# Kernel tuning notes

Measured on AMD Instinct MI355X. Metric: run time of the kernel, lower is better.

The kernel has to match this reference:

```python
import jax, jax.numpy as jnp
import numpy as np

N_UNITS = 1024
H = 16
D_HEAD = N_UNITS // H
D_FF = 4 * N_UNITS
BATCH = 8
SEQ = 1024
EPS = 1e-3


def setup_inputs() -> dict:
    key = jax.random.key(0)
    ks = jax.random.split(key, 12)
    s = 3.0 / N_UNITS  # LinearSent init scale (not math-relevant, just realistic)
    sf = 3.0 / D_FF
    return {
        "e": jax.random.normal(ks[0], (BATCH, N_UNITS, SEQ), dtype=jnp.float32),
        "xx_mask": jnp.ones((BATCH, SEQ, SEQ), dtype=bool),
        "W_Q": jax.random.uniform(ks[1], (N_UNITS, N_UNITS), minval=-s, maxval=s),
        "W_K": jax.random.uniform(ks[2], (N_UNITS, N_UNITS), minval=-s, maxval=s),
        "W_V": jax.random.uniform(ks[3], (N_UNITS, N_UNITS), minval=-s, maxval=s),
        "W_O": jax.random.uniform(ks[4], (N_UNITS, N_UNITS), minval=-s, maxval=s),
        "W_1": jax.random.uniform(ks[5], (D_FF, N_UNITS), minval=-s, maxval=s),
        "b_1": jnp.zeros((D_FF,), dtype=jnp.float32),
        "W_2": jax.random.uniform(ks[6], (N_UNITS, D_FF), minval=-sf, maxval=sf),
        "b_2": jnp.zeros((N_UNITS,), dtype=jnp.float32),
        "ln1_a": jnp.ones((N_UNITS,), dtype=jnp.float32),
        "ln1_b": jnp.zeros((N_UNITS,), dtype=jnp.float32),
        "ln2_a": jnp.ones((N_UNITS,), dtype=jnp.float32),
        "ln2_b": jnp.zeros((N_UNITS,), dtype=jnp.float32),
    }


def _layer_norm_sent(z, a, b):
    # z: (B, U, L). Torch LayerNorm normalizes over dim=1 (units) with
    # unbiased std: (z - mu) / (std + eps) * a + b
    mu = jnp.mean(z, axis=1, keepdims=True)
    sigma = jnp.std(z, axis=1, keepdims=True, ddof=1)
    return (z - mu) / (sigma + EPS) * a[None, :, None] + b[None, :, None]


def _mha(e, mask, W_Q, W_K, W_V, W_O):
    b, u, L = e.shape
    scale = 1.0 / np.sqrt(D_HEAD)
    # projections: (B, U, L); chunk along units into H heads of D_HEAD
    Q = jnp.einsum("ou,bul->bol", W_Q, e).reshape(b, H, D_HEAD, L)
    K = jnp.einsum("ou,bul->bol", W_K, e).reshape(b, H, D_HEAD, L)
    V = jnp.einsum("ou,bul->bol", W_V, e).reshape(b, H, D_HEAD, L)
    scores = jnp.einsum("bhdq,bhdk->bhqk", Q, K) * scale
    scores = jnp.where(mask[:, None, :, :], scores, -jnp.inf)
    A = jax.nn.softmax(scores, axis=-1)
    A = jnp.where(jnp.isnan(A), 0.0, A)  # fully-masked rows -> 0 (as in torch)
    C = jnp.einsum("bhqk,bhdk->bhdq", A, V).reshape(b, u, L)
    return jnp.einsum("ou,bul->bol", W_O, C)


def reference(e, xx_mask, W_Q, W_K, W_V, W_O, W_1, b_1, W_2, b_2,
              ln1_a, ln1_b, ln2_a, ln2_b):
    # self-attention + residual + LayerNormSent (dropout = identity in eval)
    e = e + _mha(e, xx_mask, W_Q, W_K, W_V, W_O)
    e = _layer_norm_sent(e, ln1_a, ln1_b)
    # position-wise FFN: W_2 @ relu(W_1 @ e + b_1) + b_2
    h = jax.nn.relu(jnp.einsum("fu,bul->bfl", W_1, e) + b_1[None, :, None])
    ffn = jnp.einsum("uf,bfl->bul", W_2, h) + b_2[None, :, None]
    e = e + ffn
    e = _layer_norm_sent(e, ln2_a, ln2_b)
    return e
```

## Files before the change

kernel.cpp:

```cpp
#include <hip/hip_runtime.h>
#include <stdint.h>

typedef float f32x4 __attribute__((ext_vector_type(4)));
typedef short s16x8 __attribute__((ext_vector_type(8)));
typedef short s16x4 __attribute__((ext_vector_type(4)));

#define B_  8
#define U_  1024
#define L_  1024
#define H_  16
#define DH_ 64
#define FF_ 4096
#define EPS_ 1e-3f

__device__ __forceinline__ short f2bf(float f){
  union { float f; uint32_t u; } x; x.f = f;
  uint32_t r = x.u + 0x7fffu + ((x.u >> 16) & 1u);
  return (short)(r >> 16);
}

__device__ __forceinline__ float bf2f(short s){
  union { uint32_t u; float f; } x; x.u = ((uint32_t)(uint16_t)s) << 16;
  return x.f;
}

__device__ __forceinline__ uint32_t cvtpk(float lo, float hi){
  uint32_t r;
  asm("v_cvt_pk_bf16_f32 %0, %1, %2" : "=v"(r) : "v"(lo), "v"(hi));
  return r;
}

__global__ __launch_bounds__(256) void castk(const float* __restrict__ in,
                                             short* __restrict__ out, int n4){
  int i = blockIdx.x * 256 + threadIdx.x;
  if (i < n4){
    f32x4 v = ((const f32x4*)in)[i];
    s16x4 o;
    o[0]=f2bf(v[0]); o[1]=f2bf(v[1]); o[2]=f2bf(v[2]); o[3]=f2bf(v[3]);
    ((s16x4*)out)[i] = o;
  }
}

__global__ __launch_bounds__(256) void transpose_e(const float* __restrict__ e,
                                                   short* __restrict__ etb){
  __shared__ float tile[32][33];
  int b = blockIdx.z;
  int u0 = blockIdx.x * 32, l0 = blockIdx.y * 32;
  int tx = threadIdx.x & 31, ty = threadIdx.x >> 5;
  const float* src = e + ((size_t)b * U_ + u0) * L_ + l0;
  #pragma unroll
  for (int k = 0; k < 32; k += 8) tile[ty + k][tx] = src[(size_t)(ty + k) * L_ + tx];
  __syncthreads();
  short* dstb = etb + ((size_t)b * L_ + l0) * U_ + u0;
  #pragma unroll
  for (int k = 0; k < 32; k += 8)
    dstb[(size_t)(ty + k) * U_ + tx] = f2bf(tile[tx][ty + k]);
}

__device__ __forceinline__ void gload16(const void* g, void* l){
  __builtin_amdgcn_global_load_lds((const __attribute__((address_space(1))) void*)g,
                                   (__attribute__((address_space(3))) void*)l, 16, 0, 0);
}

template<int MODE>
__global__ __launch_bounds__(256)
void gemm_bt(const short* __restrict__ A, int lda, long long strideA,
             const short* __restrict__ Bt, int ldb, long long strideB,
             int K,
             void* __restrict__ Out, int ldo, long long strideO)
{
  int b = blockIdx.z;
  const short* Ab = A  + (size_t)b * strideA;
  const short* Bb = Bt + (size_t)b * strideB;
  int m0 = blockIdx.x * 128, n0 = blockIdx.y * 128;
  __shared__ short As[128 * 64];
  __shared__ short Bs[128 * 64];
  int tid = threadIdx.x;
  int lane = tid & 63, wid = tid >> 6;
  int wm = (wid >> 1) * 64, wn = (wid & 1) * 64;
  int r16 = lane & 15, g4 = lane >> 4;
  f32x4 acc[4][4] = {};

  for (int k0 = 0; k0 < K; k0 += 64) {
    #pragma unroll
    for (int it = 0; it < 4; ++it) {
      int idx = it * 256 + tid;
      int row = idx >> 3, c8 = idx & 7;
      int gc = c8 ^ (row & 7);
      gload16(Ab + (size_t)(m0 + row) * lda + k0 + gc * 8, &As[idx * 8]);
    }
    #pragma unroll
    for (int it = 0; it < 4; ++it) {
      int idx = it * 256 + tid;
      int row = idx >> 3, c8 = idx & 7;
      int gc = c8 ^ (row & 7);
      gload16(Bb + (size_t)(n0 + row) * ldb + k0 + gc * 8, &Bs[idx * 8]);
    }
    __syncthreads();

    s16x8 af[4][2], bf[4][2];
    #pragma unroll
    for (int m = 0; m < 4; ++m)
      #pragma unroll
      for (int s = 0; s < 2; ++s){
        int row = wm + m * 16 + r16;
        int c = (s * 4 + g4) ^ (row & 7);
        af[m][s] = *(const s16x8*)&As[row * 64 + c * 8];
      }
    #pragma unroll
    for (int n = 0; n < 4; ++n)
      #pragma unroll
      for (int s = 0; s < 2; ++s){
        int row = wn + n * 16 + r16;
        int c = (s * 4 + g4) ^ (row & 7);
        bf[n][s] = *(const s16x8*)&Bs[row * 64 + c * 8];
      }
    #pragma unroll
    for (int m = 0; m < 4; ++m)
      #pragma unroll
      for (int n = 0; n < 4; ++n)
        #pragma unroll
        for (int s = 0; s < 2; ++s)
          acc[m][n] = __builtin_amdgcn_mfma_f32_16x16x32_bf16(af[m][s], bf[n][s], acc[m][n], 0, 0, 0);
    __syncthreads();
  }

  #pragma unroll
  for (int m = 0; m < 4; ++m)
    #pragma unroll
    for (int n = 0; n < 4; ++n)
      #pragma unroll
      for (int r = 0; r < 4; ++r){
        int gr = m0 + wm + m * 16 + g4 * 4 + r;
        int gc = n0 + wn + n * 16 + r16;
        ((short*)Out)[(size_t)b * strideO + (size_t)gr * ldo + gc] = f2bf(acc[m][n][r]);
      }
}

__device__ __forceinline__ void stage_half8(const short* __restrict__ A,
    const short* __restrict__ Bt, int lda, int ldb, int m0, int n0, int k0,
    short* As, short* Bs, int H, int tid)
{
  const short* src; short* dst; int ld, gbase;
  if (H < 2){ src = A;  dst = As + H * 128 * 64; ld = lda; gbase = m0 + H * 128; }
  else      { src = Bt; dst = Bs + (H - 2) * 128 * 64; ld = ldb; gbase = n0 + (H - 2) * 128; }
  #pragma unroll
  for (int j = 0; j < 2; ++j){
    int idx = j * 512 + tid;
    int rl = idx >> 3, c8 = idx & 7;
    int gc = c8 ^ (rl & 7);
    gload16(src + (size_t)(gbase + rl) * ld + k0 + gc * 8, dst + idx * 8);
  }
}

#define RAWBAR() asm volatile("s_barrier" ::: "memory")
#define VMCNT2() asm volatile("s_waitcnt vmcnt(2)" ::: "memory")

template<int MODE>
__global__ __launch_bounds__(512, 2)
void gemm8(const short* __restrict__ A, int lda,
           const short* __restrict__ Bt, int ldb, int K,
           void* __restrict__ Out, int ldo,
           const float* __restrict__ bias, int NTL)
{
  __shared__ short As[2][256 * 64];
  __shared__ short Bs[2][256 * 64];
  int id = blockIdx.x;
  int xcd = id & 7, j = id >> 3;
  int nt = j & ((1 << NTL) - 1);
  int mt = xcd * 4 + (j >> NTL);
  int m0 = mt * 256, n0 = nt * 256;
  int tid = threadIdx.x, lane = tid & 63, wid = tid >> 6;
  int wr = wid >> 2, wc = wid & 3;
  int r16 = lane & 15, g4 = lane >> 4;
  int NT = K >> 6;

  f32x4 acc[8][4] = {};

  stage_half8(A, Bt, lda, ldb, m0, n0, 0,  (short*)As[0], (short*)Bs[0], 0, tid);
  stage_half8(A, Bt, lda, ldb, m0, n0, 0,  (short*)As[0], (short*)Bs[0], 1, tid);
  stage_half8(A, Bt, lda, ldb, m0, n0, 0,  (short*)As[0], (short*)Bs[0], 2, tid);
  stage_half8(A, Bt, lda, ldb, m0, n0, 0,  (short*)As[0], (short*)Bs[0], 3, tid);
  stage_half8(A, Bt, lda, ldb, m0, n0, 64, (short*)As[1], (short*)Bs[1], 0, tid);
  VMCNT2();
  RAWBAR();

  for (int t = 0; t < NT; ++t){
    int c = t & 1;
    short* Asc = (short*)As[c];     short* Bsc = (short*)Bs[c];
    short* Asn = (short*)As[c ^ 1]; short* Bsn = (short*)Bs[c ^ 1];
    int kn1 = (t + 1) << 6, kn2 = (t + 2) << 6;
    bool h1 = (t + 1 < NT), h2 = (t + 2 < NT);
    s16x8 af[8], bfr[4];

    #pragma unroll
    for (int m = 0; m < 8; ++m){
      int row = wr * 128 + m * 16 + r16;
      af[m] = *(const s16x8*)&Asc[row * 64 + (g4 ^ (row & 7)) * 8];
    }
    #pragma unroll
    for (int n = 0; n < 4; ++n){
      int row = wc * 64 + n * 16 + r16;
      bfr[n] = *(const s16x8*)&Bsc[row * 64 + (g4 ^ (row & 7)) * 8];
    }
    if (h1) stage_half8(A, Bt, lda, ldb, m0, n0, kn1, Asn, Bsn, 1, tid);
    RAWBAR();
    __builtin_amdgcn_s_setprio(1);
    #pragma unroll
    for (int m = 0; m < 8; ++m){
      acc[m][0] = __builtin_amdgcn_mfma_f32_16x16x32_bf16(af[m], bfr[0], acc[m][0], 0, 0, 0);
      acc[m][1] = __builtin_amdgcn_mfma_f32_16x16x32_bf16(af[m], bfr[1], acc[m][1], 0, 0, 0);
    }
    __builtin_amdgcn_s_setprio(0);
    RAWBAR();

    if (h1) stage_half8(A, Bt, lda, ldb, m0, n0, kn1, Asn, Bsn, 2, tid);
    RAWBAR();
    __builtin_amdgcn_s_setprio(1);
    #pragma unroll
    for (int m = 0; m < 8; ++m){
      acc[m][2] = __builtin_amdgcn_mfma_f32_16x16x32_bf16(af[m], bfr[2], acc[m][2], 0, 0, 0);
      acc[m][3] = __builtin_amdgcn_mfma_f32_16x16x32_bf16(af[m], bfr[3], acc[m][3], 0, 0, 0);
    }
    __builtin_amdgcn_s_setprio(0);
    RAWBAR();

    #pragma unroll
    for (int m = 0; m < 8; ++m){
      int row = wr * 128 + m * 16 + r16;
      af[m] = *(const s16x8*)&Asc[row * 64 + ((4 + g4) ^ (row & 7)) * 8];
    }
    #pragma unroll
    for (int n = 0; n < 4; ++n){
      int row = wc * 64 + n * 16 + r16;
      bfr[n] = *(const s16x8*)&Bsc[row * 64 + ((4 + g4) ^ (row & 7)) * 8];
    }
    if (h1) stage_half8(A, Bt, lda, ldb, m0, n0, kn1, Asn, Bsn, 3, tid);
    RAWBAR();
    __builtin_amdgcn_s_setprio(1);
    #pragma unroll
    for (int m = 0; m < 8; ++m){
      acc[m][0] = __builtin_amdgcn_mfma_f32_16x16x32_bf16(af[m], bfr[0], acc[m][0], 0, 0, 0);
      acc[m][1] = __builtin_amdgcn_mfma_f32_16x16x32_bf16(af[m], bfr[1], acc[m][1], 0, 0, 0);
    }
    __builtin_amdgcn_s_setprio(0);
    RAWBAR();

    if (h2) stage_half8(A, Bt, lda, ldb, m0, n0, kn2, Asc, Bsc, 0, tid);
    RAWBAR();
    __builtin_amdgcn_s_setprio(1);
    #pragma unroll
    for (int m = 0; m < 8; ++m){
      acc[m][2] = __builtin_amdgcn_mfma_f32_16x16x32_bf16(af[m], bfr[2], acc[m][2], 0, 0, 0);
      acc[m][3] = __builtin_amdgcn_mfma_f32_16x16x32_bf16(af[m], bfr[3], acc[m][3], 0, 0, 0);
    }
    __builtin_amdgcn_s_setprio(0);
    VMCNT2();
    RAWBAR();
  }

  #pragma unroll
  for (int m = 0; m < 8; ++m)
    #pragma unroll
    for (int n = 0; n < 4; ++n)
      #pragma unroll
      for (int r = 0; r < 4; ++r){
        int gr = m0 + wr * 128 + m * 16 + g4 * 4 + r;
        int gc = n0 + wc * 64 + n * 16 + r16;
        float v = acc[m][n][r];
        if (MODE == 0){
          ((short*)Out)[(size_t)gr * ldo + gc] = f2bf(v);
        } else {
          float z = v + bias[gc]; z = z > 0.f ? z : 0.f;
          ((short*)Out)[(size_t)gr * ldo + gc] = f2bf(z);
        }
      }
}

__device__ __forceinline__ void stage_n(const short* __restrict__ A,
    const short* __restrict__ Bt, int lda, int ldb, int m0, int n0, int k0,
    short* As, short* Bs, int H, int tid)
{
  const short* src; short* dst; int ld, gbase;
  if (H < 2){ src = A;  dst = As + H * 128 * 64; ld = lda; gbase = m0 + H * 128; }
  else      { src = Bt; dst = Bs; ld = ldb; gbase = n0; }
  #pragma unroll
  for (int j = 0; j < 2; ++j){
    int idx = j * 512 + tid;
    int rl = idx >> 3, c8 = idx & 7;
    int gc = c8 ^ (rl & 7);
    gload16(src + (size_t)(gbase + rl) * ld + k0 + gc * 8, dst + idx * 8);
  }
}

template<int MODE>
__global__ __launch_bounds__(512, 2)
void gemm8n(const short* __restrict__ A, int lda,
            const short* __restrict__ Bt, int ldb, int K,
            float* __restrict__ Out, int ldo,
            const float* __restrict__ bias,
            const short* __restrict__ resb, int ldr, int NTL)
{
  __shared__ short As[2][256 * 64];
  __shared__ short Bs[2][128 * 64];
  int id = blockIdx.x;
  int xcd = id & 7, j = id >> 3;
  int nt = j & ((1 << NTL) - 1);
  int mt = xcd * 4 + (j >> NTL);
  int m0 = mt * 256, n0 = nt * 128;
  int tid = threadIdx.x, lane = tid & 63, wid = tid >> 6;
  int wr = wid >> 1, wc = wid & 1;
  int r16 = lane & 15, g4 = lane >> 4;
  int NT = K >> 6;

  f32x4 acc[4][4] = {};

  stage_n(A, Bt, lda, ldb, m0, n0, 0,  (short*)As[0], (short*)Bs[0], 0, tid);
  stage_n(A, Bt, lda, ldb, m0, n0, 0,  (short*)As[0], (short*)Bs[0], 1, tid);
  stage_n(A, Bt, lda, ldb, m0, n0, 0,  (short*)As[0], (short*)Bs[0], 2, tid);
  stage_n(A, Bt, lda, ldb, m0, n0, 64, (short*)As[1], (short*)Bs[1], 0, tid);
  VMCNT2();
  RAWBAR();

  for (int t = 0; t < NT; ++t){
    int c = t & 1;
    short* Asc = (short*)As[c];     short* Bsc = (short*)Bs[c];
    short* Asn = (short*)As[c ^ 1]; short* Bsn = (short*)Bs[c ^ 1];
    int kn1 = (t + 1) << 6, kn2 = (t + 2) << 6;
    bool h1 = (t + 1 < NT), h2 = (t + 2 < NT);
    s16x8 af[4], bfr[4];

    #pragma unroll
    for (int m = 0; m < 4; ++m){
      int row = wr * 64 + m * 16 + r16;
      af[m] = *(const s16x8*)&Asc[row * 64 + (g4 ^ (row & 7)) * 8];
    }
    #pragma unroll
    for (int n = 0; n < 4; ++n){
      int row = wc * 64 + n * 16 + r16;
      bfr[n] = *(const s16x8*)&Bsc[row * 64 + (g4 ^ (row & 7)) * 8];
    }
    if (h1) stage_n(A, Bt, lda, ldb, m0, n0, kn1, Asn, Bsn, 1, tid);
    RAWBAR();
    __builtin_amdgcn_s_setprio(1);
    #pragma unroll
    for (int m = 0; m < 4; ++m){
      acc[m][0] = __builtin_amdgcn_mfma_f32_16x16x32_bf16(af[m], bfr[0], acc[m][0], 0, 0, 0);
      acc[m][1] = __builtin_amdgcn_mfma_f32_16x16x32_bf16(af[m], bfr[1], acc[m][1], 0, 0, 0);
    }
    __builtin_amdgcn_s_setprio(0);
    RAWBAR();

    if (h1) stage_n(A, Bt, lda, ldb, m0, n0, kn1, Asn, Bsn, 2, tid);
    RAWBAR();
    __builtin_amdgcn_s_setprio(1);
    #pragma unroll
    for (int m = 0; m < 4; ++m){
      acc[m][2] = __builtin_amdgcn_mfma_f32_16x16x32_bf16(af[m], bfr[2], acc[m][2], 0, 0, 0);
      acc[m][3] = __builtin_amdgcn_mfma_f32_16x16x32_bf16(af[m], bfr[3], acc[m][3], 0, 0, 0);
    }
    __builtin_amdgcn_s_setprio(0);
    RAWBAR();

    #pragma unroll
    for (int m = 0; m < 4; ++m){
      int row = wr * 64 + m * 16 + r16;
      af[m] = *(const s16x8*)&Asc[row * 64 + ((4 + g4) ^ (row & 7)) * 8];
    }
    #pragma unroll
    for (int n = 0; n < 4; ++n){
      int row = wc * 64 + n * 16 + r16;
      bfr[n] = *(const s16x8*)&Bsc[row * 64 + ((4 + g4) ^ (row & 7)) * 8];
    }
    RAWBAR();
    __builtin_amdgcn_s_setprio(1);
    #pragma unroll
    for (int m = 0; m < 4; ++m){
      acc[m][0] = __builtin_amdgcn_mfma_f32_16x16x32_bf16(af[m], bfr[0], acc[m][0], 0, 0, 0);
      acc[m][1] = __builtin_amdgcn_mfma_f32_16x16x32_bf16(af[m], bfr[1], acc[m][1], 0, 0, 0);
    }
    __builtin_amdgcn_s_setprio(0);
    RAWBAR();

    if (h2) stage_n(A, Bt, lda, ldb, m0, n0, kn2, Asc, Bsc, 0, tid);
    RAWBAR();
    __builtin_amdgcn_s_setprio(1);
    #pragma unroll
    for (int m = 0; m < 4; ++m){
      acc[m][2] = __builtin_amdgcn_mfma_f32_16x16x32_bf16(af[m], bfr[2], acc[m][2], 0, 0, 0);
      acc[m][3] = __builtin_amdgcn_mfma_f32_16x16x32_bf16(af[m], bfr[3], acc[m][3], 0, 0, 0);
    }
    __builtin_amdgcn_s_setprio(0);
    VMCNT2();
    RAWBAR();
  }

  #pragma unroll
  for (int m = 0; m < 4; ++m)
    #pragma unroll
    for (int n = 0; n < 4; ++n)
      #pragma unroll
      for (int r = 0; r < 4; ++r){
        int gr = m0 + wr * 64 + m * 16 + g4 * 4 + r;
        int gc = n0 + wc * 64 + n * 16 + r16;
        float v = acc[m][n][r];
        float rv = bf2f(resb[(size_t)gr * ldr + gc]);
        if (MODE == 1){
          Out[(size_t)gr * ldo + gc] = v + rv;
        } else {
          Out[(size_t)gr * ldo + gc] = v + bias[gc] + rv;
        }
      }
}

__global__ __launch_bounds__(256)
void attn_kernel(const short* __restrict__ QKt,
                 const short* __restrict__ Vd, short* __restrict__ Ct)
{
  int bh = blockIdx.x;
  int b = bh >> 4, h = bh & 15;
  int qt = blockIdx.y;
  int tid = threadIdx.x, lane = tid & 63, w = tid >> 6;
  int r16 = lane & 15, g4 = lane >> 4;
  int hd = h * 64;
  const float cs = 0.125f * 1.44269504089f;
  const int LDQ = 2048;

  __shared__ short Ks[2][64 * 64];
  __shared__ short Vs[2][64 * 64];

  const short* Qb = QKt + (size_t)b * L_ * LDQ;
  const short* Kb = Qb + 1024;
  const short* Vb = Vd + (size_t)b * U_ * L_;

  s16x8 aq[2][2];
  #pragma unroll
  for (int m = 0; m < 2; ++m)
    #pragma unroll
    for (int s = 0; s < 2; ++s){
      int qrow = qt * 128 + w * 32 + m * 16 + r16;
      aq[m][s] = *(const s16x8*)&Qb[(size_t)qrow * LDQ + hd + s * 32 + g4 * 8];
    }

  f32x4 o[2][4] = {};
  float mr[2] = {0.f, 0.f};
  float lr[2] = {0.f, 0.f};

  int srow = tid >> 3, sc8 = tid & 7;
  int sgc0 = sc8 ^ (srow & 7);
  int srow1 = (256 + tid) >> 3;
  int sgc1 = sc8 ^ (srow1 & 7);

  #define STAGE(buf, kb_) do {                                                  \
    int k0s = (kb_) * 64;                                                       \
    gload16(Kb + (size_t)(k0s + srow ) * LDQ + hd + sgc0 * 8, &Ks[buf][(tid      ) * 8]); \
    gload16(Kb + (size_t)(k0s + srow1) * LDQ + hd + sgc1 * 8, &Ks[buf][(256 + tid) * 8]); \
    gload16(Vb + (size_t)(hd + srow ) * L_ + k0s + sgc0 * 8, &Vs[buf][(tid      ) * 8]); \
    gload16(Vb + (size_t)(hd + srow1) * L_ + k0s + sgc1 * 8, &Vs[buf][(256 + tid) * 8]); \
  } while (0)

  STAGE(0, 0);
  __syncthreads();
  int cur = 0;

  int a_lo = (((lane >> 4) & 1) << 7) + ((lane & 15) << 2);

  for (int kb = 0; kb < 16; ++kb){
    if (kb + 1 < 16) STAGE(cur ^ 1, kb + 1);

    s16x8 ak[4][2];
    #pragma unroll
    for (int nt = 0; nt < 4; ++nt)
      #pragma unroll
      for (int s = 0; s < 2; ++s){
        int row = nt * 16 + r16;
        int c = (s * 4 + g4) ^ (row & 7);
        ak[nt][s] = *(const s16x8*)&Ks[cur][row * 64 + c * 8];
      }
    f32x4 st[2][4];
    __builtin_amdgcn_s_setprio(1);
    #pragma unroll
    for (int m = 0; m < 2; ++m)
      #pragma unroll
      for (int nt = 0; nt < 4; ++nt){
        f32x4 a = {};
        #pragma unroll
        for (int s = 0; s < 2; ++s)
          a = __builtin_amdgcn_mfma_f32_16x16x32_bf16(ak[nt][s], aq[m][s], a, 0, 0, 0);
        st[m][nt] = a;
      }
    __builtin_amdgcn_s_setprio(0);

    s16x8 bv[4][2];
    #pragma unroll
    for (int nt2 = 0; nt2 < 4; ++nt2)
      #pragma unroll
      for (int s = 0; s < 2; ++s){
        int row = nt2 * 16 + r16;
        int c = (s * 4 + g4) ^ (row & 7);
        bv[nt2][s] = *(const s16x8*)&Vs[cur][row * 64 + c * 8];
      }

    #pragma unroll
    for (int m = 0; m < 2; ++m){
      float t0 = fmaxf(fmaxf(st[m][0][0], st[m][0][1]), fmaxf(st[m][0][2], st[m][0][3]));
      float t1 = fmaxf(fmaxf(st[m][1][0], st[m][1][1]), fmaxf(st[m][1][2], st[m][1][3]));
      float t2 = fmaxf(fmaxf(st[m][2][0], st[m][2][1]), fmaxf(st[m][2][2], st[m][2][3]));
      float t3 = fmaxf(fmaxf(st[m][3][0], st[m][3][1]), fmaxf(st[m][3][2], st[m][3][3]));
      float tmax = fmaxf(fmaxf(t0, t1), fmaxf(t2, t3));

      if (!__all(tmax <= mr[m] + 64.f)){
        float tf = tmax;
        tf = fmaxf(tf, __shfl_xor(tf, 16, 64));
        tf = fmaxf(tf, __shfl_xor(tf, 32, 64));
        float mn = fmaxf(mr[m], tf);
        float alpha = exp2f((mr[m] - mn) * cs);
        mr[m] = mn;
        lr[m] *= alpha;
        float ar[4];
        #pragma unroll
        for (int r = 0; r < 4; ++r)
          ar[r] = __shfl(alpha, (lane & 48) | ((((lane >> 4) & 3) * 4 + r) & 15), 64);
        #pragma unroll
        for (int nt2 = 0; nt2 < 4; ++nt2)
          #pragma unroll
          for (int r = 0; r < 4; ++r) o[m][nt2][r] *= ar[r];
      }

      float m2 = mr[m] * cs;
      float p[4][4], ps = 0.f;
      #pragma unroll
      for (int nt = 0; nt < 4; ++nt)
        #pragma unroll
        for (int r = 0; r < 4; ++r){
          float pv = exp2f(st[m][nt][r] * cs - m2);
          p[nt][r] = pv;
          ps += pv;
        }
      lr[m] += ps;

      uint32_t pw[4][2];
      #pragma unroll
      for (int nt = 0; nt < 4; ++nt){
        pw[nt][0] = cvtpk(p[nt][0], p[nt][1]);
        pw[nt][1] = cvtpk(p[nt][2], p[nt][3]);
      }
      union { uint32_t w[4]; s16x8 v; } pa[2];
      #pragma unroll
      for (int s = 0; s < 2; ++s)
        #pragma unroll
        for (int wj = 0; wj < 4; ++wj){
          int addr = a_lo + ((wj >> 1) << 6);
          uint32_t A  = __builtin_amdgcn_ds_bpermute(addr, (int)pw[2 * s    ][wj & 1]);
          uint32_t Bv = __builtin_amdgcn_ds_bpermute(addr, (int)pw[2 * s + 1][wj & 1]);
          pa[s].w[wj] = (lane < 32) ? A : Bv;
        }

      __builtin_amdgcn_s_setprio(1);
      #pragma unroll
      for (int s = 0; s < 2; ++s)
        #pragma unroll
        for (int nt2 = 0; nt2 < 4; ++nt2)
          o[m][nt2] = __builtin_amdgcn_mfma_f32_16x16x32_bf16(pa[s].v, bv[nt2][s], o[m][nt2], 0, 0, 0);
      __builtin_amdgcn_s_setprio(0);
    }

    __syncthreads();
    cur ^= 1;
  }
  #undef STAGE

  short* Cb = Ct + (size_t)b * L_ * U_;
  #pragma unroll
  for (int m = 0; m < 2; ++m){
    float l = lr[m];
    l += __shfl_xor(l, 16, 64);
    l += __shfl_xor(l, 32, 64);
    float linv = 1.f / l;
    float lv[4];
    #pragma unroll
    for (int r = 0; r < 4; ++r)
      lv[r] = __shfl(linv, (lane & 48) | ((((lane >> 4) & 3) * 4 + r) & 15), 64);
    #pragma unroll
    for (int nt2 = 0; nt2 < 4; ++nt2)
      #pragma unroll
      for (int r = 0; r < 4; ++r){
        int q = qt * 128 + w * 32 + m * 16 + g4 * 4 + r;
        float v = o[m][nt2][r] * lv[r];
        Cb[(size_t)q * U_ + hd + nt2 * 16 + r16] = f2bf(v);
      }
  }
}

__global__ __launch_bounds__(256)
void ln_kernel(const float* __restrict__ z, const float* __restrict__ ga,
               const float* __restrict__ gb, short* __restrict__ outb)
{
  int row = blockIdx.x;
  const float* zr = z + (size_t)row * U_;
  int tid = threadIdx.x;
  float v[4];
  float s = 0.f, sq = 0.f;
  #pragma unroll
  for (int i = 0; i < 4; ++i){
    v[i] = zr[tid + i * 256];
    s += v[i]; sq += v[i] * v[i];
  }
  #pragma unroll
  for (int d = 1; d < 64; d <<= 1){
    s  += __shfl_xor(s, d, 64);
    sq += __shfl_xor(sq, d, 64);
  }
  __shared__ float ss[4], ssq[4];
  int w = tid >> 6, lane = tid & 63;
  if (lane == 0){ ss[w] = s; ssq[w] = sq; }
  __syncthreads();
  s  = ss[0] + ss[1] + ss[2] + ss[3];
  sq = ssq[0] + ssq[1] + ssq[2] + ssq[3];
  float mu = s * (1.f / 1024.f);
  float var = (sq - 1024.f * mu * mu) * (1.f / 1023.f);
  var = var > 0.f ? var : 0.f;
  float inv = 1.f / (sqrtf(var) + EPS_);
  #pragma unroll
  for (int i = 0; i < 4; ++i){
    int u = tid + i * 256;
    outb[(size_t)row * U_ + u] = f2bf((v[i] - mu) * inv * ga[u] + gb[u]);
  }
}

__global__ __launch_bounds__(256)
void ln_stats(const float* __restrict__ z, float* __restrict__ st2)
{
  int row = blockIdx.x;
  const float* zr = z + (size_t)row * U_;
  int tid = threadIdx.x;
  float s = 0.f, sq = 0.f;
  #pragma unroll
  for (int i = 0; i < 4; ++i){
    float v = zr[tid + i * 256];
    s += v; sq += v * v;
  }
  #pragma unroll
  for (int d = 1; d < 64; d <<= 1){
    s  += __shfl_xor(s, d, 64);
    sq += __shfl_xor(sq, d, 64);
  }
  __shared__ float ss[4], ssq[4];
  int w = tid >> 6, lane = tid & 63;
  if (lane == 0){ ss[w] = s; ssq[w] = sq; }
  __syncthreads();
  if (tid == 0){
    s  = ss[0] + ss[1] + ss[2] + ss[3];
    sq = ssq[0] + ssq[1] + ssq[2] + ssq[3];
    float mu = s * (1.f / 1024.f);
    float var = (sq - 1024.f * mu * mu) * (1.f / 1023.f);
    var = var > 0.f ? var : 0.f;
    st2[2 * row]     = mu;
    st2[2 * row + 1] = 1.f / (sqrtf(var) + EPS_);
  }
}

__global__ __launch_bounds__(256)
void transpose_ln(const float* __restrict__ z, const float* __restrict__ st2,
                  const float* __restrict__ ga, const float* __restrict__ gb,
                  float* __restrict__ out)
{
  __shared__ float tile[32][33];
  int b = blockIdx.z;
  int l0 = blockIdx.x * 32, u0 = blockIdx.y * 32;
  int tx = threadIdx.x & 31, ty = threadIdx.x >> 5;
  const float* src = z + ((size_t)b * L_ + l0) * U_ + u0;
  #pragma unroll
  for (int k = 0; k < 32; k += 8) tile[ty + k][tx] = src[(size_t)(ty + k) * U_ + tx];
  __syncthreads();
  size_t rbase = (size_t)b * L_ + l0 + tx;
  float mu  = st2[2 * rbase];
  float inv = st2[2 * rbase + 1];
  float* dst = out + ((size_t)b * U_ + u0) * L_ + l0;
  #pragma unroll
  for (int k = 0; k < 32; k += 8){
    int u = u0 + ty + k;
    float v = (tile[tx][ty + k] - mu) * inv * ga[u] + gb[u];
    dst[(size_t)(ty + k) * L_ + tx] = v;
  }
}

extern "C" void kernel_launch(void* const* d_in, const int* in_sizes, int n_in,
                              void* d_out, int out_size, void* d_ws, size_t ws_size,
                              hipStream_t stream)
{
  const float* e    = (const float*)d_in[0];
  const float* W_Q  = (const float*)d_in[2];
  const float* W_K  = (const float*)d_in[3];
  const float* W_V  = (const float*)d_in[4];
  const float* W_O  = (const float*)d_in[5];
  const float* W_1  = (const float*)d_in[6];
  const float* b_1  = (const float*)d_in[7];
  const float* W_2  = (const float*)d_in[8];
  const float* b_2  = (const float*)d_in[9];
  const float* ln1a = (const float*)d_in[10];
  const float* ln1b = (const float*)d_in[11];
  const float* ln2a = (const float*)d_in[12];
  const float* ln2b = (const float*)d_in[13];

  char* ws = (char*)d_ws;
  const size_t MB = 1ull << 20;
  short* wbqk = (short*)(ws + 0 * MB);
  short* wbv  = (short*)(ws + 4 * MB);
  short* wbo  = (short*)(ws + 6 * MB);
  short* wb1  = (short*)(ws + 8 * MB);
  short* wb2  = (short*)(ws + 16 * MB);
  short* etb  = (short*)(ws + 24 * MB);
  float* st2  = (float*)(ws + 56 * MB);
  short* QKt  = (short*)(ws + 72 * MB);
  short* Vd   = (short*)(ws + 104 * MB);
  short* Ct   = (short*)(ws + 120 * MB);
  float* z1t  = (float*)(ws + 72 * MB);
  short* e1b  = (short*)(ws + 104 * MB);
  short* ht   = (short*)(ws + 136 * MB);
  float* z2t  = (float*)(ws + 24 * MB);

  const long long S1M = 1024LL * 1024LL;

  castk<<<1024, 256, 0, stream>>>(W_Q, wbqk, 262144);
  castk<<<1024, 256, 0, stream>>>(W_K, wbqk + 1048576, 262144);
  castk<<<1024, 256, 0, stream>>>(W_V, wbv, 262144);
  castk<<<1024, 256, 0, stream>>>(W_O, wbo, 262144);
  castk<<<4096, 256, 0, stream>>>(W_1, wb1, 1048576);
  castk<<<4096, 256, 0, stream>>>(W_2, wb2, 1048576);

  transpose_e<<<dim3(32, 32, 8), 256, 0, stream>>>(e, etb);

  gemm8<0><<<256, 512, 0, stream>>>(etb, 1024, wbqk, 1024, 1024, QKt, 2048,
                                    nullptr, 3);
  gemm_bt<0><<<dim3(8, 8, 8), 256, 0, stream>>>(wbv, 1024, 0, etb, 1024, S1M, 1024,
                                                Vd, 1024, S1M);

  attn_kernel<<<dim3(128, 8), 256, 0, stream>>>(QKt, Vd, Ct);

  gemm8n<1><<<256, 512, 0, stream>>>(Ct, 1024, wbo, 1024, 1024, z1t, 1024,
                                     nullptr, etb, 1024, 3);
  ln_kernel<<<8192, 256, 0, stream>>>(z1t, ln1a, ln1b, e1b);

  gemm8<2><<<512, 512, 0, stream>>>(e1b, 1024, wb1, 1024, 1024, ht, 4096,
                                    b_1, 4);
  gemm8n<3><<<256, 512, 0, stream>>>(ht, 4096, wb2, 4096, 4096, z2t, 1024,
                                     b_2, e1b, 1024, 3);

  ln_stats<<<8192, 256, 0, stream>>>(z2t, st2);
  transpose_ln<<<dim3(32, 32, 8), 256, 0, stream>>>(z2t, st2, ln2a, ln2b, (float*)d_out);
}
```

Before: 401.6 us.

## Replace V-projection GEMM with pipelined 256x128 kernel and fuse weight casts

The V projection used a simple 128x128 GEMM that staged each k-tile and then synchronised before computing. It is replaced with a 512-thread 256x128 tile kernel that double-buffers LDS through async global-to-LDS loads interleaved with MFMA phases, uses setprio around MFMAs, and orders blocks with XCD-aware indexing. The six separate weight-cast launches are merged into one kernel to cut launch overhead. The new kernel adds more barriers and relies on a stage_n helper defined elsewhere in the file.

Result: faster. 390.8 us (-2.7%).

```diff
diff --git a/kernel.cpp b/kernel.cpp
--- a/kernel.cpp
+++ b/kernel.cpp
@@ -30,15 +30,28 @@
   return r;
 }
 
-__global__ __launch_bounds__(256) void castk(const float* __restrict__ in,
-                                             short* __restrict__ out, int n4){
+__global__ __launch_bounds__(256)
+void castall(const float* __restrict__ wq, const float* __restrict__ wk,
+             const float* __restrict__ wv, const float* __restrict__ wo,
+             const float* __restrict__ w1, const float* __restrict__ w2,
+             short* __restrict__ wbqk, short* __restrict__ wbv,
+             short* __restrict__ wbo, short* __restrict__ wb1,
+             short* __restrict__ wb2)
+{
   int i = blockIdx.x * 256 + threadIdx.x;
-  if (i < n4){
-    f32x4 v = ((const f32x4*)in)[i];
-    s16x4 o;
-    o[0]=f2bf(v[0]); o[1]=f2bf(v[1]); o[2]=f2bf(v[2]); o[3]=f2bf(v[3]);
-    ((s16x4*)out)[i] = o;
-  }
+  const float* src; short* dst; int off;
+  if (i < 524288){
+    if (i < 262144){ src = wq; dst = wbqk;            off = i; }
+    else           { src = wk; dst = wbqk + 1048576;  off = i - 262144; }
+  } else if (i < 1048576){
+    if (i < 786432){ src = wv; dst = wbv; off = i - 524288; }
+    else           { src = wo; dst = wbo; off = i - 786432; }
+  } else if (i < 2097152){ src = w1; dst = wb1; off = i - 1048576; }
+  else                   { src = w2; dst = wb2; off = i - 2097152; }
+  f32x4 v = ((const f32x4*)src)[off];
+  s16x4 o;
+  o[0]=f2bf(v[0]); o[1]=f2bf(v[1]); o[2]=f2bf(v[2]); o[3]=f2bf(v[3]);
+  ((s16x4*)dst)[off] = o;
 }
 
 __global__ __launch_bounds__(256) void transpose_e(const float* __restrict__ e,
@@ -62,80 +75,8 @@
                                    (__attribute__((address_space(3))) void*)l, 16, 0, 0);
 }
 
-template<int MODE>
-__global__ __launch_bounds__(256)
-void gemm_bt(const short* __restrict__ A, int lda, long long strideA,
-             const short* __restrict__ Bt, int ldb, long long strideB,
-             int K,
-             void* __restrict__ Out, int ldo, long long strideO)
-{
-  int b = blockIdx.z;
-  const short* Ab = A  + (size_t)b * strideA;
-  const short* Bb = Bt + (size_t)b * strideB;
-  int m0 = blockIdx.x * 128, n0 = blockIdx.y * 128;
-  __shared__ short As[128 * 64];
-  __shared__ short Bs[128 * 64];
-  int tid = threadIdx.x;
-  int lane = tid & 63, wid = tid >> 6;
-  int wm = (wid >> 1) * 64, wn = (wid & 1) * 64;
-  int r16 = lane & 15, g4 = lane >> 4;
-  f32x4 acc[4][4] = {};
-
-  for (int k0 = 0; k0 < K; k0 += 64) {
-    #pragma unroll
-    for (int it = 0; it < 4; ++it) {
-      int idx = it * 256 + tid;
-      int row = idx >> 3, c8 = idx & 7;
-      int gc = c8 ^ (row & 7);
-      gload16(Ab + (size_t)(m0 + row) * lda + k0 + gc * 8, &As[idx * 8]);
-    }
-    #pragma unroll
-    for (int it = 0; it < 4; ++it) {
-      int idx = it * 256 + tid;
-      int row = idx >> 3, c8 = idx & 7;
-      int gc = c8 ^ (row & 7);
-      gload16(Bb + (size_t)(n0 + row) * ldb + k0 + gc * 8, &Bs[idx * 8]);
-    }
-    __syncthreads();
-
-    s16x8 af[4][2], bf[4][2];
-    #pragma unroll
-    for (int m = 0; m < 4; ++m)
-      #pragma unroll
-      for (int s = 0; s < 2; ++s){
-        int row = wm + m * 16 + r16;
-        int c = (s * 4 + g4) ^ (row & 7);
-        af[m][s] = *(const s16x8*)&As[row * 64 + c * 8];
-      }
-    #pragma unroll
-    for (int n = 0; n < 4; ++n)
-      #pragma unroll
-      for (int s = 0; s < 2; ++s){
-        int row = wn + n * 16 + r16;
-        int c = (s * 4 + g4) ^ (row & 7);
-        bf[n][s] = *(const s16x8*)&Bs[row * 64 + c * 8];
-      }
-    #pragma unroll
-    for (int m = 0; m < 4; ++m)
-      #pragma unroll
-      for (int n = 0; n < 4; ++n)
-        #pragma unroll
-        for (int s = 0; s < 2; ++s)
-          acc[m][n] = __builtin_amdgcn_mfma_f32_16x16x32_bf16(af[m][s], bf[n][s], acc[m][n], 0, 0, 0);
-    __syncthreads();
-  }
-
-  #pragma unroll
-  for (int m = 0; m < 4; ++m)
-    #pragma unroll
-    for (int n = 0; n < 4; ++n)
-      #pragma unroll
-      for (int r = 0; r < 4; ++r){
-        int gr = m0 + wm + m * 16 + g4 * 4 + r;
-        int gc = n0 + wn + n * 16 + r16;
-        ((short*)Out)[(size_t)b * strideO + (size_t)gr * ldo + gc] = f2bf(acc[m][n][r]);
-      }
-}
+#define RAWBAR() asm volatile("s_barrier" ::: "memory")
+#define VMCNT2() asm volatile("s_waitcnt vmcnt(2)" ::: "memory")
 
 __device__ __forceinline__ void stage_half8(const short* __restrict__ A,
     const short* __restrict__ Bt, int lda, int ldb, int m0, int n0, int k0,
@@ -152,9 +93,6 @@
     gload16(src + (size_t)(gbase + rl) * ld + k0 + gc * 8, dst + idx * 8);
   }
 }
-
-#define RAWBAR() asm volatile("s_barrier" ::: "memory")
-#define VMCNT2() asm volatile("s_waitcnt vmcnt(2)" ::: "memory")
 
 template<int MODE>
 __global__ __launch_bounds__(512, 2)
@@ -410,6 +348,120 @@
         } else {
           Out[(size_t)gr * ldo + gc] = v + bias[gc] + rv;
         }
+      }
+}
+
+__global__ __launch_bounds__(512, 2)
+void gemm8b(const short* __restrict__ A,
+            const short* __restrict__ Bt,
+            short* __restrict__ Out)
+{
+  __shared__ short As[2][256 * 64];
+  __shared__ short Bs[2][128 * 64];
+  int id = blockIdx.x;
+  int xcd = id & 7, j = id >> 3;
+  int pair = xcd * 8 + (j >> 2);
+  int mt = j & 3;
+  int b = pair >> 3, nt = pair & 7;
+  int m0 = mt * 256, n0 = nt * 128;
+  const short* Bb = Bt + (size_t)b * 1048576;
+  short* Ob = Out + (size_t)b * 1048576;
+  int tid = threadIdx.x, lane = tid & 63, wid = tid >> 6;
+  int wr = wid >> 1, wc = wid & 1;
+  int r16 = lane & 15, g4 = lane >> 4;
+  const int NT = 16;
+
+  f32x4 acc[4][4] = {};
+
+  stage_n(A, Bb, 1024, 1024, m0, n0, 0,  (short*)As[0], (short*)Bs[0], 0, tid);
+  stage_n(A, Bb, 1024, 1024, m0, n0, 0,  (short*)As[0], (short*)Bs[0], 1, tid);
+  stage_n(A, Bb, 1024, 1024, m0, n0, 0,  (short*)As[0], (short*)Bs[0], 2, tid);
+  stage_n(A, Bb, 1024, 1024, m0, n0, 64, (short*)As[1], (short*)Bs[1], 0, tid);
+  VMCNT2();
+  RAWBAR();
+
+  for (int t = 0; t < NT; ++t){
+    int c = t & 1;
+    short* Asc = (short*)As[c];     short* Bsc = (short*)Bs[c];
+    short* Asn = (short*)As[c ^ 1]; short* Bsn = (short*)Bs[c ^ 1];
+    int kn1 = (t + 1) << 6, kn2 = (t + 2) << 6;
+    bool h1 = (t + 1 < NT), h2 = (t + 2 < NT);
+    s16x8 af[4], bfr[4];
+
+    #pragma unroll
+    for (int m = 0; m < 4; ++m){
+      int row = wr * 64 + m * 16 + r16;
+      af[m] = *(const s16x8*)&Asc[row * 64 + (g4 ^ (row & 7)) * 8];
+    }
+    #pragma unroll
+    for (int n = 0; n < 4; ++n){
+      int row = wc * 64 + n * 16 + r16;
+      bfr[n] = *(const s16x8*)&Bsc[row * 64 + (g4 ^ (row & 7)) * 8];
+    }
+    if (h1) stage_n(A, Bb, 1024, 1024, m0, n0, kn1, Asn, Bsn, 1, tid);
+    RAWBAR();
+    __builtin_amdgcn_s_setprio(1);
+    #pragma unroll
+    for (int m = 0; m < 4; ++m){
+      acc[m][0] = __builtin_amdgcn_mfma_f32_16x16x32_bf16(af[m], bfr[0], acc[m][0], 0, 0, 0);
+      acc[m][1] = __builtin_amdgcn_mfma_f32_16x16x32_bf16(af[m], bfr[1], acc[m][1], 0, 0, 0);
+    }
+    __builtin_amdgcn_s_setprio(0);
+    RAWBAR();
+
+    if (h1) stage_n(A, Bb, 1024, 1024, m0, n0, kn1, Asn, Bsn, 2, tid);
+    RAWBAR();
+    __builtin_amdgcn_s_setprio(1);
+    #pragma unroll
+    for (int m = 0; m < 4; ++m){
+      acc[m][2] = __builtin_amdgcn_mfma_f32_16x16x32_bf16(af[m], bfr[2], acc[m][2], 0, 0, 0);
+      acc[m][3] = __builtin_amdgcn_mfma_f32_16x16x32_bf16(af[m], bfr[3], acc[m][3], 0, 0, 0);
+    }
+    __builtin_amdgcn_s_setprio(0);
+    RAWBAR();
+
+    #pragma unroll
+    for (int m = 0; m < 4; ++m){
+      int row = wr * 64 + m * 16 + r16;
+      af[m] = *(const s16x8*)&Asc[row * 64 + ((4 + g4) ^ (row & 7)) * 8];
+    }
+    #pragma unroll
+    for (int n = 0; n < 4; ++n){
+      int row = wc * 64 + n * 16 + r16;
+      bfr[n] = *(const s16x8*)&Bsc[row * 64 + ((4 + g4) ^ (row & 7)) * 8];
+    }
+    RAWBAR();
+    __builtin_amdgcn_s_setprio(1);
+    #pragma unroll
+    for (int m = 0; m < 4; ++m){
+      acc[m][0] = __builtin_amdgcn_mfma_f32_16x16x32_bf16(af[m], bfr[0], acc[m][0], 0, 0, 0);
+      acc[m][1] = __builtin_amdgcn_mfma_f32_16x16x32_bf16(af[m], bfr[1], acc[m][1], 0, 0, 0);
+    }
+    __builtin_amdgcn_s_setprio(0);
+    RAWBAR();
+
+    if (h2) stage_n(A, Bb, 1024, 1024, m0, n0, kn2, Asc, Bsc, 0, tid);
+    RAWBAR();
+    __builtin_amdgcn_s_setprio(1);
+    #pragma unroll
+    for (int m = 0; m < 4; ++m){
+      acc[m][2] = __builtin_amdgcn_mfma_f32_16x16x32_bf16(af[m], bfr[2], acc[m][2], 0, 0, 0);
+      acc[m][3] = __builtin_amdgcn_mfma_f32_16x16x32_bf16(af[m], bfr[3], acc[m][3], 0, 0, 0);
+    }
+    __builtin_amdgcn_s_setprio(0);
+    VMCNT2();
+    RAWBAR();
+  }
+
+  #pragma unroll
+  for (int m = 0; m < 4; ++m)
+    #pragma unroll
+    for (int n = 0; n < 4; ++n)
+      #pragma unroll
+      for (int r = 0; r < 4; ++r){
+        int gr = m0 + wr * 64 + m * 16 + g4 * 4 + r;
+        int gc = n0 + wc * 64 + n * 16 + r16;
+        Ob[(size_t)gr * 1024 + gc] = f2bf(acc[m][n][r]);
       }
 }
 
@@ -720,21 +772,14 @@
   short* ht   = (short*)(ws + 136 * MB);
   float* z2t  = (float*)(ws + 24 * MB);
 
-  const long long S1M = 1024LL * 1024LL;
-
-  castk<<<1024, 256, 0, stream>>>(W_Q, wbqk, 262144);
-  castk<<<1024, 256, 0, stream>>>(W_K, wbqk + 1048576, 262144);
-  castk<<<1024, 256, 0, stream>>>(W_V, wbv, 262144);
-  castk<<<1024, 256, 0, stream>>>(W_O, wbo, 262144);
-  castk<<<4096, 256, 0, stream>>>(W_1, wb1, 1048576);
-  castk<<<4096, 256, 0, stream>>>(W_2, wb2, 1048576);
+  castall<<<12288, 256, 0, stream>>>(W_Q, W_K, W_V, W_O, W_1, W_2,
+                                     wbqk, wbv, wbo, wb1, wb2);
 
   transpose_e<<<dim3(32, 32, 8), 256, 0, stream>>>(e, etb);
 
   gemm8<0><<<256, 512, 0, stream>>>(etb, 1024, wbqk, 1024, 1024, QKt, 2048,
                                     nullptr, 3);
-  gemm_bt<0><<<dim3(8, 8, 8), 256, 0, stream>>>(wbv, 1024, 0, etb, 1024, S1M, 1024,
-                                                Vd, 1024, S1M);
+  gemm8b<<<256, 512, 0, stream>>>(wbv, etb, Vd);
 
   attn_kernel<<<dim3(128, 8), 256, 0, stream>>>(QKt, Vd, Ct);
 
```
